# Optimization experiments

Hardware: AMD Instinct MI355X
Metric: run time of the kernel (lower is better)

Reference implementation:

```python
import jax, jax.numpy as jnp
import numpy as np

B, C_IN, C_OUT, H, W = 8, 256, 256, 48, 48


def setup_inputs() -> dict:
    key = jax.random.key(0)
    ks = jax.random.split(key, 8)
    s = 1.0 / np.sqrt(C_IN)
    return {
        "x1": jax.random.normal(ks[0], (B, C_IN, H, W), dtype=jnp.float32),
        "x2": jax.random.normal(ks[1], (B, C_IN, H, W), dtype=jnp.float32),
        "Wq": jax.random.normal(ks[2], (C_OUT, C_IN), dtype=jnp.float32) * s,
        "bq": jax.random.normal(ks[3], (C_OUT,), dtype=jnp.float32) * s,
        "Wk": jax.random.normal(ks[4], (C_OUT, C_IN), dtype=jnp.float32) * s,
        "bk": jax.random.normal(ks[5], (C_OUT,), dtype=jnp.float32) * s,
        "Wv": jax.random.normal(ks[6], (C_OUT, C_IN), dtype=jnp.float32) * s,
        "bv": jax.random.normal(ks[7], (C_OUT,), dtype=jnp.float32) * s,
    }


def _conv1x1(x, Wt, b):
    # x: [B,Cin,H,W], Wt: [Cout,Cin] -> [B,Cout,H,W]
    return jnp.einsum("bchw,oc->bohw", x, Wt) + b[None, :, None, None]


def reference(x1, x2, Wq, bq, Wk, bk, Wv, bv):
    q = _conv1x1(x1, Wq, bq)  # [B,C,H,W]
    k = _conv1x1(x2, Wk, bk)
    v = _conv1x1(x2, Wv, bv)
    b, c, h, w = q.shape
    n = h * w
    qf = q.reshape(b, c, n).transpose(0, 2, 1)  # [B,N,C]
    kf = k.reshape(b, c, n)                      # [B,C,N]
    vf = v.reshape(b, c, n).transpose(0, 2, 1)   # [B,N,C]
    # NOTE: faithful to source -- no 1/sqrt(d) scaling, no head split
    attn = jax.nn.softmax(jnp.einsum("bic,bcj->bij", qf, kf), axis=-1)  # [B,N,N]
    out = jnp.einsum("bij,bjc->bic", attn, vf)   # [B,N,C]
    return out.transpose(0, 2, 1).reshape(b, c, h, w)
```

## Files before the change

### kernel.cpp

```cpp
#include <hip/hip_runtime.h>
#include <cfloat>
#include <cstddef>
#include <cstdint>

#define BATCH 8
#define CDIM  256
#define NTOK  2304

typedef float    f32x4 __attribute__((ext_vector_type(4)));
typedef _Float16 f16x8 __attribute__((ext_vector_type(8)));
typedef _Float16 f16x4 __attribute__((ext_vector_type(4)));

#define MFMA16(a, b, c) __builtin_amdgcn_mfma_f32_16x16x32_f16(a, b, c, 0, 0, 0)

__device__ __forceinline__ void gl_lds16(const void* g, void* l) {
    __builtin_amdgcn_global_load_lds(
        (const __attribute__((address_space(1))) void*)g,
        (__attribute__((address_space(3))) void*)l, 16, 0, 0);
}

__global__ __launch_bounds__(256) void cast_w(
    const float* __restrict__ Wq, const float* __restrict__ Wk,
    const float* __restrict__ Wv, _Float16* __restrict__ Wh)
{
    int i = (blockIdx.x * 256 + threadIdx.x) * 4;
    const float* src = (i < 65536) ? (Wq + i)
                     : (i < 131072) ? (Wk + (i - 65536)) : (Wv + (i - 131072));
    float4 v = *(const float4*)src;
    f16x4 h = { (_Float16)v.x, (_Float16)v.y, (_Float16)v.z, (_Float16)v.w };
    *(f16x4*)(Wh + i) = h;
}

__global__ __launch_bounds__(256) void cast_x(
    const float* __restrict__ x1, const float* __restrict__ x2,
    _Float16* __restrict__ Xt1, _Float16* __restrict__ Xt2)
{
    const int tid = threadIdx.x;
    const int n0 = blockIdx.x * 64;
    const int c0 = blockIdx.y * 64;
    const int bz = blockIdx.z;
    const float* X   = (bz < 8) ? x1 : x2;
    _Float16*   Xt   = (bz < 8) ? Xt1 : Xt2;
    const int b = bz & 7;

    __shared__ _Float16 T[64][72];

    {
        const int cl = tid >> 2, nch = (tid & 3) * 16;
        const float* src = X + (size_t)(b * CDIM + c0 + cl) * NTOK + n0 + nch;
#pragma unroll
        for (int u = 0; u < 4; ++u) {
            float4 v = *(const float4*)(src + u * 4);
            T[cl][nch + u * 4 + 0] = (_Float16)v.x;
            T[cl][nch + u * 4 + 1] = (_Float16)v.y;
            T[cl][nch + u * 4 + 2] = (_Float16)v.z;
            T[cl][nch + u * 4 + 3] = (_Float16)v.w;
        }
    }
    __syncthreads();
    {
        const int nl = tid >> 2, cch = (tid & 3) * 16;
        _Float16* dst = Xt + (size_t)(b * NTOK + n0 + nl) * CDIM + c0 + cch;
        f16x8 o0, o1;
#pragma unroll
        for (int i = 0; i < 8; ++i) {
            o0[i] = T[cch + i][nl];
            o1[i] = T[cch + 8 + i][nl];
        }
        *(f16x8*)dst = o0;
        *(f16x8*)(dst + 8) = o1;
    }
}

__global__ __launch_bounds__(256, 2) void proj_mfma(
    const _Float16* __restrict__ Xt1, const _Float16* __restrict__ Xt2,
    const _Float16* __restrict__ Wh,
    const float* __restrict__ bq, const float* __restrict__ bk,
    const float* __restrict__ bv,
    _Float16* __restrict__ Qo, _Float16* __restrict__ Ko, _Float16* __restrict__ Vo)
{
    const int tid  = threadIdx.x;
    const int lane = tid & 63;
    const int w    = tid >> 6;
    const int l15  = lane & 15, l4 = lane >> 4;
    const int n0   = blockIdx.x * 64;
    const int mode = blockIdx.y;
    const int b    = blockIdx.z;

    const _Float16* Xt = (mode == 0) ? Xt1 : Xt2;
    const _Float16* Wm = Wh + mode * 65536;
    const float* bias  = (mode == 0) ? bq : (mode == 1) ? bk : bv;
    _Float16* OUT      = (mode == 0) ? Qo : (mode == 1) ? Ko : Vo;

    __shared__ __align__(16) char sm[65536];
    _Float16* Xl = (_Float16*)sm;
    _Float16* Wl = (_Float16*)(sm + 32768);

#pragma unroll
    for (int t = 0; t < 8; ++t) {
        int i = w * 8 + t;
        int row = 2 * i + (lane >> 5);
        int ch  = lane & 31;
        gl_lds16(Xt + (size_t)(b * NTOK + n0 + row) * CDIM + ((ch ^ (row & 7)) * 8),
                 (char*)Xl + i * 1024);
    }

    float bias_o[4];
#pragma unroll
    for (int ot = 0; ot < 4; ++ot) bias_o[ot] = bias[w * 64 + ot * 16 + l15];

    f32x4 acc[16];
#pragma unroll
    for (int i = 0; i < 16; ++i) acc[i] = (f32x4){0.f, 0.f, 0.f, 0.f};

    for (int c0 = 0; c0 < CDIM; c0 += 64) {
        __syncthreads();
#pragma unroll
        for (int t = 0; t < 8; ++t) {
            int i = w * 8 + t;
            int row = 8 * i + (lane >> 3);
            int ch  = lane & 7;
            gl_lds16(Wm + (size_t)row * CDIM + c0 + ((ch ^ (row & 7)) * 8),
                     (char*)Wl + i * 1024);
        }
        __syncthreads();

#pragma unroll
        for (int kk2 = 0; kk2 < 2; ++kk2) {
            f16x8 a[4], bf[4];
#pragma unroll
            for (int nt = 0; nt < 4; ++nt) {
                int row = nt * 16 + l15;
                int ch  = ((c0 >> 3) + kk2 * 4 + l4) ^ (row & 7);
                a[nt] = *(const f16x8*)((const char*)Xl + row * 512 + ch * 16);
            }
#pragma unroll
            for (int ot = 0; ot < 4; ++ot) {
                int row = w * 64 + ot * 16 + l15;
                int ch  = (kk2 * 4 + l4) ^ (row & 7);
                bf[ot] = *(const f16x8*)((const char*)Wl + row * 128 + ch * 16);
            }
#pragma unroll
            for (int nt = 0; nt < 4; ++nt)
#pragma unroll
                for (int ot = 0; ot < 4; ++ot)
                    acc[nt * 4 + ot] = MFMA16(a[nt], bf[ot], acc[nt * 4 + ot]);
        }
    }

    __syncthreads();

    if (mode <= 1) {
        _Float16* Dl = (_Float16*)sm;
#pragma unroll
        for (int nt = 0; nt < 4; ++nt)
#pragma unroll
            for (int ot = 0; ot < 4; ++ot)
#pragma unroll
                for (int reg = 0; reg < 4; ++reg)
                    Dl[(nt * 16 + 4 * l4 + reg) * 256 + w * 64 + ot * 16 + l15] =
                        (_Float16)(acc[nt * 4 + ot][reg] + bias_o[ot]);
        __syncthreads();
        char* dst = (char*)(OUT + ((size_t)b * NTOK + n0) * CDIM);
#pragma unroll
        for (int u = 0; u < 8; ++u) {
            f16x8 v = *(const f16x8*)((const char*)Dl + u * 4096 + tid * 16);
            *(f16x8*)(dst + u * 4096 + tid * 16) = v;
        }
    } else {
        _Float16* Dlv = (_Float16*)sm;
#pragma unroll
        for (int nt = 0; nt < 4; ++nt)
#pragma unroll
            for (int ot = 0; ot < 4; ++ot)
#pragma unroll
                for (int reg = 0; reg < 4; ++reg)
                    Dlv[(w * 64 + ot * 16 + l15) * 80 + nt * 16 + 4 * l4 + reg] =
                        (_Float16)(acc[nt * 4 + ot][reg] + bias_o[ot]);
        __syncthreads();
#pragma unroll
        for (int t = 0; t < 8; ++t) {
            int ro = (w * 8 + t) * 8 + (lane >> 3);
            f16x8 v = *(const f16x8*)((const char*)Dlv + ro * 160 + (lane & 7) * 16);
            *(f16x8*)(OUT + ((size_t)b * CDIM + ro) * NTOK + n0 + (lane & 7) * 8) = v;
        }
    }
}

template <int SEG>
__global__ __launch_bounds__(512, 2) void attn_fa(
    const _Float16* __restrict__ Q, const _Float16* __restrict__ K,
    const _Float16* __restrict__ Vt, _Float16* __restrict__ pacc,
    float2* __restrict__ pml)
{
    const int tid  = threadIdx.x;
    const int lane = tid & 63;
    const int w    = tid >> 6;
    const int l15  = lane & 15, l4 = lane >> 4;

    const int nb  = 18 * BATCH * SEG, cpx = nb / 8;
    const int bid = blockIdx.x;
    const int swz = (bid & 7) * cpx + (bid >> 3);
    const int x = swz % 18;
    const int b = (swz / 18) & 7;
    const int z = swz / 144;

    const int row0   = x * 128 + w * 16;
    const int jbase  = z * (NTOK / SEG);
    const int NTILES = NTOK / SEG / 64;

    __shared__ __align__(16) char smem[131072];

    const size_t kbb = (size_t)b * NTOK;
    const size_t vbb = (size_t)b * CDIM * NTOK;

    auto stage = [&](int j0, int buf) {
        char* Klc = smem + buf * 65536;
        char* Vlc = Klc + 32768;
#pragma unroll
        for (int t = 0; t < 4; ++t) {
            int i  = w * 4 + t;
            int lr = 2 * i + (lane >> 5);
            int gr = (lr & 32) | ((lr & 12) << 1) | ((lr & 16) >> 2) | (lr & 3);
            int chunk = lane & 31;
            gl_lds16(K + (kbb + j0 + gr) * CDIM + ((chunk ^ (lr & 7)) * 8),
                     Klc + i * 1024);
        }
#pragma unroll
        for (int t = 0; t < 4; ++t) {
            int i = w * 4 + t;
            int vrow = 8 * i + (lane >> 3);
            int chunk = lane & 7;
            gl_lds16(Vt + vbb + (size_t)vrow * NTOK + j0 + ((chunk ^ (vrow & 7)) * 8),
                     Vlc + i * 1024);
        }
    };

    f16x8 qa[8];
    {
        const _Float16* qb = Q + ((size_t)b * NTOK + row0 + l15) * CDIM + l4 * 8;
#pragma unroll
        for (int kk = 0; kk < 8; ++kk)
            qa[kk] = __builtin_nontemporal_load((const f16x8*)(qb + kk * 32));
    }

    f32x4 acc[16];
#pragma unroll
    for (int ct = 0; ct < 16; ++ct) acc[ct] = (f32x4){0.f, 0.f, 0.f, 0.f};
    f32x4 accl = (f32x4){0.f, 0.f, 0.f, 0.f};
    float m = -FLT_MAX;

    const f16x8 vone = {(_Float16)1.f, (_Float16)1.f, (_Float16)1.f, (_Float16)1.f,
                        (_Float16)1.f, (_Float16)1.f, (_Float16)1.f, (_Float16)1.f};

    stage(jbase, 0);
    __syncthreads();

    for (int jt = 0; jt < NTILES; ++jt) {
        const int cur = jt & 1;

        if (jt + 1 < NTILES) stage(jbase + (jt + 1) * 64, cur ^ 1);

        const char* Klc = (const char*)smem + cur * 65536;
        const char* Vlc = Klc + 32768;

        f32x4 s[4];
#pragma unroll
        for (int nt = 0; nt < 4; ++nt) {
            const char* kb = Klc + (nt * 16 + l15) * 512;
            f32x4 sv = (f32x4){0.f, 0.f, 0.f, 0.f};
#pragma unroll
            for (int kk = 0; kk < 8; ++kk) {
                f16x8 kf = *(const f16x8*)(kb + (((kk * 4 + l4) ^ (l15 & 7)) * 16));
                sv = MFMA16(kf, qa[kk], sv);
            }
            s[nt] = sv;
        }

        float pm = fmaxf(fmaxf(s[0][0], s[0][1]), fmaxf(s[0][2], s[0][3]));
        pm = fmaxf(pm, fmaxf(fmaxf(s[1][0], s[1][1]), fmaxf(s[1][2], s[1][3])));
        pm = fmaxf(pm, fmaxf(fmaxf(s[2][0], s[2][1]), fmaxf(s[2][2], s[2][3])));
        pm = fmaxf(pm, fmaxf(fmaxf(s[3][0], s[3][1]), fmaxf(s[3][2], s[3][3])));
        pm = fmaxf(pm, __shfl_xor(pm, 16));
        pm = fmaxf(pm, __shfl_xor(pm, 32));
        if (pm > m + 8.f) {
            float sc = __expf(m - pm);
            m = pm;
#pragma unroll
            for (int e = 0; e < 4; ++e) accl[e] *= sc;
#pragma unroll
            for (int ct = 0; ct < 16; ++ct)
#pragma unroll
                for (int e = 0; e < 4; ++e) acc[ct][e] *= sc;
        }

        f16x8 pa[2];
#pragma unroll
        for (int kc = 0; kc < 2; ++kc)
#pragma unroll
            for (int e = 0; e < 8; ++e)
                pa[kc][e] = (_Float16)__expf(s[2 * kc + (e >> 2)][e & 3] - m);

        accl = MFMA16(vone, pa[0], accl);
        accl = MFMA16(vone, pa[1], accl);
#pragma unroll
        for (int ct = 0; ct < 16; ++ct) {
            const char* vb0 = Vlc + (ct * 16 + l15) * 128;
#pragma unroll
            for (int kc = 0; kc < 2; ++kc) {
                f16x8 vb = *(const f16x8*)(vb0 + (((kc * 4 + l4) ^ (l15 & 7)) * 16));
                acc[ct] = MFMA16(vb, pa[kc], acc[ct]);
            }
        }

        __syncthreads();
    }

    _Float16* stg = (_Float16*)(smem + w * 8448);
    {
        float inv = 1.f / accl[0];
#pragma unroll
        for (int ct = 0; ct < 16; ++ct) {
            f16x4 o = { (_Float16)(acc[ct][0] * inv), (_Float16)(acc[ct][1] * inv),
                        (_Float16)(acc[ct][2] * inv), (_Float16)(acc[ct][3] * inv) };
            *(f16x4*)&stg[l15 * 264 + ct * 16 + l4 * 4] = o;
        }
        if (l4 == 0)
            pml[((size_t)z * BATCH + b) * NTOK + row0 + l15] =
                make_float2(m, accl[0]);
    }
    asm volatile("s_waitcnt lgkmcnt(0)" ::: "memory");
    __builtin_amdgcn_sched_barrier(0);
    {
        const char* stgc = (const char*)stg;
        char* dst = (char*)(pacc + ((size_t)z * BATCH + b) * NTOK * CDIM
                            + (size_t)row0 * CDIM);
#pragma unroll
        for (int u = 0; u < 8; ++u) {
            int r = 2 * u + (lane >> 5);
            f16x8 v = *(const f16x8*)(stgc + r * 528 + (lane & 31) * 16);
            *(f16x8*)(dst + r * 512 + (lane & 31) * 16) = v;
        }
    }
}

template <int SEG>
__global__ __launch_bounds__(256) void merge_kernel(
    const _Float16* __restrict__ pacc, const float2* __restrict__ pml,
    float* __restrict__ out)
{
    const int tid = threadIdx.x;
    const int n0 = blockIdx.x * 64;
    const int b  = blockIdx.y;

    __shared__ float wgt[SEG][64];
    __shared__ float dinv[64];
    __shared__ float T[64][68];

    if (tid < 64) {
        int n = n0 + tid;
        float ms[SEG], ls[SEG];
#pragma unroll
        for (int s = 0; s < SEG; ++s) {
            float2 v = pml[((size_t)s * BATCH + b) * NTOK + n];
            ms[s] = v.x; ls[s] = v.y;
        }
        float M = ms[0];
#pragma unroll
        for (int s = 1; s < SEG; ++s) M = fmaxf(M, ms[s]);
        float den = 0.f;
#pragma unroll
        for (int s = 0; s < SEG; ++s) {
            float g = ls[s] * __expf(ms[s] - M);
            wgt[s][tid] = g;
            den += g;
        }
        dinv[tid] = 1.f / den;
    }
    __syncthreads();

    for (int cc = 0; cc < 4; ++cc) {
        const int nl = tid >> 2, cg = (tid & 3) * 16;
        float a[16];
#pragma unroll
        for (int u = 0; u < 16; ++u) a[u] = 0.f;
#pragma unroll
        for (int s = 0; s < SEG; ++s) {
            const _Float16* p = pacc + (((size_t)s * BATCH + b) * NTOK + n0 + nl) * CDIM
                                + cc * 64 + cg;
            f16x8 v0 = ((const f16x8*)p)[0];
            f16x8 v1 = ((const f16x8*)p)[1];
            float g = wgt[s][nl];
#pragma unroll
            for (int u = 0; u < 8; ++u) {
                a[u]     += g * (float)v0[u];
                a[8 + u] += g * (float)v1[u];
            }
        }
        float di = dinv[nl];
#pragma unroll
        for (int u = 0; u < 16; ++u) T[nl][cg + u] = a[u] * di;
        __syncthreads();

        const int cl = tid >> 2, nb2 = (tid & 3) * 16;
        float* ob = out + ((size_t)b * CDIM + cc * 64 + cl) * NTOK + n0 + nb2;
#pragma unroll
        for (int u = 0; u < 4; ++u) {
            float4 v = { T[nb2 + u * 4 + 0][cl], T[nb2 + u * 4 + 1][cl],
                         T[nb2 + u * 4 + 2][cl], T[nb2 + u * 4 + 3][cl] };
            *(float4*)&ob[u * 4] = v;
        }
        __syncthreads();
    }
}

extern "C" void kernel_launch(void* const* d_in, const int* in_sizes, int n_in,
                              void* d_out, int out_size, void* d_ws, size_t ws_size,
                              hipStream_t stream)
{
    const float* x1 = (const float*)d_in[0];
    const float* x2 = (const float*)d_in[1];
    const float* Wq = (const float*)d_in[2];
    const float* bq = (const float*)d_in[3];
    const float* Wk = (const float*)d_in[4];
    const float* bk = (const float*)d_in[5];
    const float* Wv = (const float*)d_in[6];
    const float* bv = (const float*)d_in[7];
    float* out = (float*)d_out;

    const size_t plane = (size_t)BATCH * NTOK * CDIM;
    _Float16* ws16 = (_Float16*)d_ws;
    _Float16* Q   = ws16;
    _Float16* K   = ws16 + plane;
    _Float16* Vt  = ws16 + 2 * plane;
    _Float16* Xt1 = ws16 + 3 * plane;
    _Float16* Xt2 = ws16 + 4 * plane;
    _Float16* Wh  = ws16 + 5 * plane;
    const size_t fixed16 = 5 * plane + 196608;

    auto need = [&](size_t S) {
        return fixed16 * 2 + S * plane * 2 + S * (size_t)BATCH * NTOK * 8;
    };
    const int SEG = (ws_size >= need(3)) ? 3 : (ws_size >= need(2)) ? 2 : 1;

    _Float16* pacc = ws16 + fixed16;
    float2*   pml  = (float2*)((char*)d_ws + fixed16 * 2 + (size_t)SEG * plane * 2);

    cast_w<<<dim3(192), dim3(256), 0, stream>>>(Wq, Wk, Wv, Wh);
    cast_x<<<dim3(36, 4, 16), dim3(256), 0, stream>>>(x1, x2, Xt1, Xt2);
    proj_mfma<<<dim3(36, 3, BATCH), dim3(256), 0, stream>>>(
        Xt1, Xt2, Wh, bq, bk, bv, Q, K, Vt);

    const int nb = 18 * BATCH;
    if (SEG == 3) {
        attn_fa<3><<<dim3(nb * 3), dim3(512), 0, stream>>>(Q, K, Vt, pacc, pml);
        merge_kernel<3><<<dim3(36, BATCH), dim3(256), 0, stream>>>(pacc, pml, out);
    } else if (SEG == 2) {
        attn_fa<2><<<dim3(nb * 2), dim3(512), 0, stream>>>(Q, K, Vt, pacc, pml);
        merge_kernel<2><<<dim3(36, BATCH), dim3(256), 0, stream>>>(pacc, pml, out);
    } else {
        attn_fa<1><<<dim3(nb), dim3(512), 0, stream>>>(Q, K, Vt, pacc, pml);
        merge_kernel<1><<<dim3(36, BATCH), dim3(256), 0, stream>>>(pacc, pml, out);
    }
}
```

Measured before the change: 121.2 us.

## Process two 16-row query groups per wave to reuse K/V LDS fragments

Each wave in the flash-attention kernel now handles 32 query rows (two 16-row groups) instead of 16. Every K and V fragment read from LDS feeds two MFMAs, halving LDS read traffic per unit of work. The grid shrinks to half as many blocks, each covering 256 rows. In exchange, accumulator and Q register use doubles under a 512-thread, 2-blocks-per-CU launch bound, which risks spilling. With fewer blocks, the grid may also no longer fill every CU.

```diff
diff --git a/kernel.cpp b/kernel.cpp
--- a/kernel.cpp
+++ b/kernel.cpp
@@ -198,14 +198,14 @@
     const int w    = tid >> 6;
     const int l15  = lane & 15, l4 = lane >> 4;
 
-    const int nb  = 18 * BATCH * SEG, cpx = nb / 8;
+    const int nb  = 9 * BATCH * SEG, cpx = nb / 8;
     const int bid = blockIdx.x;
     const int swz = (bid & 7) * cpx + (bid >> 3);
-    const int x = swz % 18;
-    const int b = (swz / 18) & 7;
-    const int z = swz / 144;
-
-    const int row0   = x * 128 + w * 16;
+    const int x = swz % 9;
+    const int b = (swz / 9) & 7;
+    const int z = swz / 72;
+
+    const int row0   = x * 256 + w * 32;
     const int jbase  = z * (NTOK / SEG);
     const int NTILES = NTOK / SEG / 64;
 
@@ -236,19 +236,26 @@
         }
     };
 
-    f16x8 qa[8];
+    f16x8 qa_lo[8], qa_hi[8];
     {
         const _Float16* qb = Q + ((size_t)b * NTOK + row0 + l15) * CDIM + l4 * 8;
 #pragma unroll
-        for (int kk = 0; kk < 8; ++kk)
-            qa[kk] = __builtin_nontemporal_load((const f16x8*)(qb + kk * 32));
-    }
-
-    f32x4 acc[16];
-#pragma unroll
-    for (int ct = 0; ct < 16; ++ct) acc[ct] = (f32x4){0.f, 0.f, 0.f, 0.f};
-    f32x4 accl = (f32x4){0.f, 0.f, 0.f, 0.f};
-    float m = -FLT_MAX;
+        for (int kk = 0; kk < 8; ++kk) {
+            qa_lo[kk] = __builtin_nontemporal_load((const f16x8*)(qb + kk * 32));
+            qa_hi[kk] = __builtin_nontemporal_load(
+                            (const f16x8*)(qb + 16 * CDIM + kk * 32));
+        }
+    }
+
+    f32x4 acc_lo[16], acc_hi[16];
+#pragma unroll
+    for (int ct = 0; ct < 16; ++ct) {
+        acc_lo[ct] = (f32x4){0.f, 0.f, 0.f, 0.f};
+        acc_hi[ct] = (f32x4){0.f, 0.f, 0.f, 0.f};
+    }
+    f32x4 accl_lo = (f32x4){0.f, 0.f, 0.f, 0.f};
+    f32x4 accl_hi = (f32x4){0.f, 0.f, 0.f, 0.f};
+    float m_lo = -FLT_MAX, m_hi = -FLT_MAX;
 
     const f16x8 vone = {(_Float16)1.f, (_Float16)1.f, (_Float16)1.f, (_Float16)1.f,
                         (_Float16)1.f, (_Float16)1.f, (_Float16)1.f, (_Float16)1.f};
@@ -264,52 +271,84 @@
         const char* Klc = (const char*)smem + cur * 65536;
         const char* Vlc = Klc + 32768;
 
-        f32x4 s[4];
+        f32x4 s_lo[4], s_hi[4];
 #pragma unroll
         for (int nt = 0; nt < 4; ++nt) {
             const char* kb = Klc + (nt * 16 + l15) * 512;
-            f32x4 sv = (f32x4){0.f, 0.f, 0.f, 0.f};
+            f32x4 sl = (f32x4){0.f, 0.f, 0.f, 0.f};
+            f32x4 sh = (f32x4){0.f, 0.f, 0.f, 0.f};
 #pragma unroll
             for (int kk = 0; kk < 8; ++kk) {
                 f16x8 kf = *(const f16x8*)(kb + (((kk * 4 + l4) ^ (l15 & 7)) * 16));
-                sv = MFMA16(kf, qa[kk], sv);
-            }
-            s[nt] = sv;
-        }
-
-        float pm = fmaxf(fmaxf(s[0][0], s[0][1]), fmaxf(s[0][2], s[0][3]));
-        pm = fmaxf(pm, fmaxf(fmaxf(s[1][0], s[1][1]), fmaxf(s[1][2], s[1][3])));
-        pm = fmaxf(pm, fmaxf(fmaxf(s[2][0], s[2][1]), fmaxf(s[2][2], s[2][3])));
-        pm = fmaxf(pm, fmaxf(fmaxf(s[3][0], s[3][1]), fmaxf(s[3][2], s[3][3])));
-        pm = fmaxf(pm, __shfl_xor(pm, 16));
-        pm = fmaxf(pm, __shfl_xor(pm, 32));
-        if (pm > m + 8.f) {
-            float sc = __expf(m - pm);
-            m = pm;
-#pragma unroll
-            for (int e = 0; e < 4; ++e) accl[e] *= sc;
-#pragma unroll
-            for (int ct = 0; ct < 16; ++ct)
-#pragma unroll
-                for (int e = 0; e < 4; ++e) acc[ct][e] *= sc;
-        }
-
-        f16x8 pa[2];
-#pragma unroll
-        for (int kc = 0; kc < 2; ++kc)
-#pragma unroll
-            for (int e = 0; e < 8; ++e)
-                pa[kc][e] = (_Float16)__expf(s[2 * kc + (e >> 2)][e & 3] - m);
-
-        accl = MFMA16(vone, pa[0], accl);
-        accl = MFMA16(vone, pa[1], accl);
+                sl = MFMA16(kf, qa_lo[kk], sl);
+                sh = MFMA16(kf, qa_hi[kk], sh);
+            }
+            s_lo[nt] = sl;
+            s_hi[nt] = sh;
+        }
+
+        f16x8 pa_lo[2], pa_hi[2];
+        {
+            float pm = fmaxf(fmaxf(s_lo[0][0], s_lo[0][1]), fmaxf(s_lo[0][2], s_lo[0][3]));
+            pm = fmaxf(pm, fmaxf(fmaxf(s_lo[1][0], s_lo[1][1]), fmaxf(s_lo[1][2], s_lo[1][3])));
+            pm = fmaxf(pm, fmaxf(fmaxf(s_lo[2][0], s_lo[2][1]), fmaxf(s_lo[2][2], s_lo[2][3])));
+            pm = fmaxf(pm, fmaxf(fmaxf(s_lo[3][0], s_lo[3][1]), fmaxf(s_lo[3][2], s_lo[3][3])));
+            pm = fmaxf(pm, __shfl_xor(pm, 16));
+            pm = fmaxf(pm, __shfl_xor(pm, 32));
+            if (pm > m_lo + 8.f) {
+                float sc = __expf(m_lo - pm);
+                m_lo = pm;
+#pragma unroll
+                for (int e = 0; e < 4; ++e) accl_lo[e] *= sc;
+#pragma unroll
+                for (int ct = 0; ct < 16; ++ct)
+#pragma unroll
+                    for (int e = 0; e < 4; ++e) acc_lo[ct][e] *= sc;
+            }
+#pragma unroll
+            for (int kc = 0; kc < 2; ++kc)
+#pragma unroll
+                for (int e = 0; e < 8; ++e)
+                    pa_lo[kc][e] =
+                        (_Float16)__expf(s_lo[2 * kc + (e >> 2)][e & 3] - m_lo);
+        }
+        {
+            float pm = fmaxf(fmaxf(s_hi[0][0], s_hi[0][1]), fmaxf(s_hi[0][2], s_hi[0][3]));
+            pm = fmaxf(pm, fmaxf(fmaxf(s_hi[1][0], s_hi[1][1]), fmaxf(s_hi[1][2], s_hi[1][3])));
+            pm = fmaxf(pm, fmaxf(fmaxf(s_hi[2][0], s_hi[2][1]), fmaxf(s_hi[2][2], s_hi[2][3])));
+            pm = fmaxf(pm, fmaxf(fmaxf(s_hi[3][0], s_hi[3][1]), fmaxf(s_hi[3][2], s_hi[3][3])));
+            pm = fmaxf(pm, __shfl_xor(pm, 16));
+            pm = fmaxf(pm, __shfl_xor(pm, 32));
+            if (pm > m_hi + 8.f) {
+                float sc = __expf(m_hi - pm);
+                m_hi = pm;
+#pragma unroll
+                for (int e = 0; e < 4; ++e) accl_hi[e] *= sc;
+#pragma unroll
+                for (int ct = 0; ct < 16; ++ct)
+#pragma unroll
+                    for (int e = 0; e < 4; ++e) acc_hi[ct][e] *= sc;
+            }
+#pragma unroll
+            for (int kc = 0; kc < 2; ++kc)
+#pragma unroll
+                for (int e = 0; e < 8; ++e)
+                    pa_hi[kc][e] =
+                        (_Float16)__expf(s_hi[2 * kc + (e >> 2)][e & 3] - m_hi);
+        }
+
+        accl_lo = MFMA16(vone, pa_lo[0], accl_lo);
+        accl_lo = MFMA16(vone, pa_lo[1], accl_lo);
+        accl_hi = MFMA16(vone, pa_hi[0], accl_hi);
+        accl_hi = MFMA16(vone, pa_hi[1], accl_hi);
 #pragma unroll
         for (int ct = 0; ct < 16; ++ct) {
             const char* vb0 = Vlc + (ct * 16 + l15) * 128;
 #pragma unroll
             for (int kc = 0; kc < 2; ++kc) {
                 f16x8 vb = *(const f16x8*)(vb0 + (((kc * 4 + l4) ^ (l15 & 7)) * 16));
-                acc[ct] = MFMA16(vb, pa[kc], acc[ct]);
+                acc_lo[ct] = MFMA16(vb, pa_lo[kc], acc_lo[ct]);
+                acc_hi[ct] = MFMA16(vb, pa_hi[kc], acc_hi[ct]);
             }
         }
 
@@ -317,24 +356,50 @@
     }
 
     _Float16* stg = (_Float16*)(smem + w * 8448);
-    {
-        float inv = 1.f / accl[0];
+    const size_t pbase = ((size_t)z * BATCH + b) * NTOK * CDIM;
+    {
+        float inv = 1.f / accl_lo[0];
 #pragma unroll
         for (int ct = 0; ct < 16; ++ct) {
-            f16x4 o = { (_Float16)(acc[ct][0] * inv), (_Float16)(acc[ct][1] * inv),
-                        (_Float16)(acc[ct][2] * inv), (_Float16)(acc[ct][3] * inv) };
+            f16x4 o = { (_Float16)(acc_lo[ct][0] * inv), (_Float16)(acc_lo[ct][1] * inv),
+                        (_Float16)(acc_lo[ct][2] * inv), (_Float16)(acc_lo[ct][3] * inv) };
             *(f16x4*)&stg[l15 * 264 + ct * 16 + l4 * 4] = o;
         }
         if (l4 == 0)
             pml[((size_t)z * BATCH + b) * NTOK + row0 + l15] =
-                make_float2(m, accl[0]);
+                make_float2(m_lo, accl_lo[0]);
     }
     asm volatile("s_waitcnt lgkmcnt(0)" ::: "memory");
     __builtin_amdgcn_sched_barrier(0);
     {
         const char* stgc = (const char*)stg;
-        char* dst = (char*)(pacc + ((size_t)z * BATCH + b) * NTOK * CDIM
-                            + (size_t)row0 * CDIM);
+        char* dst = (char*)(pacc + pbase + (size_t)row0 * CDIM);
+#pragma unroll
+        for (int u = 0; u < 8; ++u) {
+            int r = 2 * u + (lane >> 5);
+            f16x8 v = *(const f16x8*)(stgc + r * 528 + (lane & 31) * 16);
+            *(f16x8*)(dst + r * 512 + (lane & 31) * 16) = v;
+        }
+    }
+    asm volatile("s_waitcnt lgkmcnt(0)" ::: "memory");
+    __builtin_amdgcn_sched_barrier(0);
+    {
+        float inv = 1.f / accl_hi[0];
+#pragma unroll
+        for (int ct = 0; ct < 16; ++ct) {
+            f16x4 o = { (_Float16)(acc_hi[ct][0] * inv), (_Float16)(acc_hi[ct][1] * inv),
+                        (_Float16)(acc_hi[ct][2] * inv), (_Float16)(acc_hi[ct][3] * inv) };
+            *(f16x4*)&stg[l15 * 264 + ct * 16 + l4 * 4] = o;
+        }
+        if (l4 == 0)
+            pml[((size_t)z * BATCH + b) * NTOK + row0 + 16 + l15] =
+                make_float2(m_hi, accl_hi[0]);
+    }
+    asm volatile("s_waitcnt lgkmcnt(0)" ::: "memory");
+    __builtin_amdgcn_sched_barrier(0);
+    {
+        const char* stgc = (const char*)stg;
+        char* dst = (char*)(pacc + pbase + (size_t)(row0 + 16) * CDIM);
 #pragma unroll
         for (int u = 0; u < 8; ++u) {
             int r = 2 * u + (lane >> 5);
@@ -451,7 +516,7 @@
     proj_mfma<<<dim3(36, 3, BATCH), dim3(256), 0, stream>>>(
         Xt1, Xt2, Wh, bq, bk, bv, Q, K, Vt);
 
-    const int nb = 18 * BATCH;
+    const int nb = 9 * BATCH;
     if (SEG == 3) {
         attn_fa<3><<<dim3(nb * 3), dim3(512), 0, stream>>>(Q, K, Vt, pacc, pml);
         merge_kernel<3><<<dim3(36, BATCH), dim3(256), 0, stream>>>(pacc, pml, out);
```

Result: slower. 147.0 us (+21.3%).
